# Kernel tuning notes

Measured on AMD Instinct MI355X. Metric: run time of the kernel, lower is better.

Reference implementation:

```python
import jax, jax.numpy as jnp
import numpy as np

N = 100000
E = 1600000
DIN = 128
H = 64
OUT_CLAMP = 10.0


def setup_inputs() -> dict:
    key = jax.random.key(0)
    ks = jax.random.split(key, 8)
    x = jax.random.normal(ks[0], (N, DIN), dtype=jnp.float32)
    edge_index = jax.random.randint(ks[1], (2, E), 0, N, dtype=jnp.int64)
    edge_weight = jax.random.uniform(ks[2], (E,), dtype=jnp.float32)
    # learned params (glorot-ish scale)
    W1 = jax.random.normal(ks[3], (DIN, H), dtype=jnp.float32) / np.sqrt(DIN)
    b1 = jnp.zeros((H,), dtype=jnp.float32)
    W2 = jax.random.normal(ks[4], (H, H), dtype=jnp.float32) / np.sqrt(H)
    b2 = jnp.zeros((H,), dtype=jnp.float32)
    fc_w = jax.random.normal(ks[5], (H, 1), dtype=jnp.float32) / np.sqrt(H)
    fc_b = jnp.zeros((1,), dtype=jnp.float32)
    return {"x": x, "edge_index": edge_index, "edge_weight": edge_weight,
            "W1": W1, "b1": b1, "W2": W2, "b2": b2, "fc_w": fc_w, "fc_b": fc_b}


def _gcn_conv(h, src, dst, norm, W, b, n_nodes):
    # h: [N, Fin] -> [N, Fout]. PyG GCNConv: linear, gather at source,
    # scale by symmetric norm, scatter-add at target, add bias.
    hw = h @ W                                   # [N, Fout]
    msg = hw[src] * norm[:, None]                # [E+N, Fout]
    out = jax.ops.segment_sum(msg, dst, num_segments=n_nodes)
    return out + b


def _gcn_norm(edge_index, edge_weight, n_nodes):
    # add self-loops with weight 1, compute deg^-1/2 symmetric norm
    loop = jnp.arange(n_nodes, dtype=edge_index.dtype)
    src = jnp.concatenate([edge_index[0], loop])
    dst = jnp.concatenate([edge_index[1], loop])
    ew = jnp.concatenate([edge_weight, jnp.ones((n_nodes,), edge_weight.dtype)])
    deg = jax.ops.segment_sum(ew, dst, num_segments=n_nodes)
    dis = jnp.where(deg > 0, jax.lax.rsqrt(jnp.maximum(deg, 1e-12)), 0.0)
    norm = dis[src] * ew * dis[dst]
    return src, dst, norm


def reference(x, edge_index, edge_weight, W1, b1, W2, b2, fc_w, fc_b):
    src, dst, norm = _gcn_norm(edge_index, edge_weight, N)
    h = _gcn_conv(x, src, dst, norm, W1, b1, N)
    h = _gcn_conv(h, src, dst, norm, W2, b2, N)
    out = h @ fc_w + fc_b                        # [N, 1]
    out = jnp.clip(out, 0.0, OUT_CLAMP)
    return jnp.round(out)
```

## Files before the change

### kernel.cpp

```cpp
#include <hip/hip_runtime.h>

#define DIN 128
#define BINW 128
#define BINSHIFT 7
#define NB_MAX 1024
#define CHUNK 8192


__global__ void precompute_kernel(const float* __restrict__ W1, const float* __restrict__ b1,
                                  const float* __restrict__ W2, const float* __restrict__ b2,
                                  const float* __restrict__ fcw, const float* __restrict__ fcb,
                                  double* __restrict__ w1f, double* __restrict__ cvals,
                                  unsigned* __restrict__ binCnt, int nb) {
    const int t = threadIdx.x;
    if (blockIdx.x > 0) {
        int i = (blockIdx.x - 1) * 256 + t;
        if (i < nb) binCnt[i] = 0u;
        return;
    }
    __shared__ double sw2f[64];
    if (t < 64) {
        double s = 0.0;
        for (int j = 0; j < 64; j++) s += (double)W2[t * 64 + j] * (double)fcw[j];
        sw2f[t] = s;
    }
    __syncthreads();
    if (t < 128) {
        double s = 0.0;
        for (int j = 0; j < 64; j++) s += (double)W1[t * 64 + j] * sw2f[j];
        w1f[t] = s;
    }
    if (t == 128) {
        double c1 = 0.0, c0 = (double)fcb[0];
        for (int j = 0; j < 64; j++) {
            c1 += (double)b1[j] * sw2f[j];
            c0 += (double)b2[j] * (double)fcw[j];
        }
        cvals[0] = c0;
        cvals[1] = c1;
    }
}

__global__ __launch_bounds__(256) void hist_gemv_kernel(
        const int* __restrict__ dst, const float* __restrict__ X,
        const double* __restrict__ w1f, unsigned* __restrict__ binCnt,
        double2* __restrict__ pk1, int n, int e, int nb, int hblk) {
    __shared__ unsigned cnt[NB_MAX];
    const int blk = blockIdx.x;
    const int t = threadIdx.x;
    if (blk < hblk) {
        for (int b = t; b < nb; b += 256) cnt[b] = 0u;
        __syncthreads();
        const long base = (long)blk * CHUNK;
        for (int k = 0; k < CHUNK / 256; k++) {
            long i = base + k * 256 + t;
            if (i < e) atomicAdd(&cnt[dst[i] >> BINSHIFT], 1u);
        }
        __syncthreads();
        for (int b = t; b < nb; b += 256) {
            unsigned c = cnt[b];
            if (c) atomicAdd(&binCnt[b], c);
        }
        return;
    }
    long g = (long)(blk - hblk) * 256 + t;
    int row = (int)(g >> 6);
    int lane = (int)(g & 63);
    if (row >= n) return;
    float2 x = *(const float2*)(X + (long)row * DIN + 2 * lane);
    double v = (double)x.x * w1f[2 * lane] + (double)x.y * w1f[2 * lane + 1];
#pragma unroll
    for (int off = 32; off > 0; off >>= 1) v += __shfl_down(v, off, 64);
    if (lane == 0) pk1[row].x = v;
}

__global__ void scan_kernel(const unsigned* __restrict__ binCnt,
                            unsigned* __restrict__ binBase,
                            unsigned* __restrict__ binCur, int nb) {
    __shared__ unsigned part[256];
    const int t = threadIdx.x;
    unsigned loc[4];
    unsigned s = 0;
#pragma unroll
    for (int k = 0; k < 4; k++) {
        int idx = t * 4 + k;
        unsigned v = (idx < nb) ? binCnt[idx] : 0u;
        loc[k] = s;
        s += v;
    }
    part[t] = s;
    __syncthreads();
    if (t == 0) {
        unsigned run = 0;
        for (int j = 0; j < 256; j++) { unsigned v = part[j]; part[j] = run; run += v; }
    }
    __syncthreads();
    unsigned p = part[t];
#pragma unroll
    for (int k = 0; k < 4; k++) {
        int idx = t * 4 + k;
        if (idx < nb) { binBase[idx] = p + loc[k]; binCur[idx] = p + loc[k]; }
    }
    if (t == 255) binBase[nb] = p + s;
}

__global__ __launch_bounds__(256) void binscatter_kernel(
        const int* __restrict__ src, const int* __restrict__ dst,
        const float* __restrict__ ew, unsigned* __restrict__ binCur,
        uint2* __restrict__ binned, int e, int nb) {
    __shared__ unsigned cnt[NB_MAX];
    __shared__ unsigned rb[NB_MAX];
    const int blk = blockIdx.x;
    const int t = threadIdx.x;
    for (int b = t; b < nb; b += 256) cnt[b] = 0u;
    __syncthreads();
    const long base = (long)blk * CHUNK;
    for (int k = 0; k < CHUNK / 256; k++) {
        long i = base + k * 256 + t;
        if (i < e) atomicAdd(&cnt[dst[i] >> BINSHIFT], 1u);
    }
    __syncthreads();
    for (int b = t; b < nb; b += 256) {
        unsigned c = cnt[b];
        rb[b] = c ? atomicAdd(&binCur[b], c) : 0u;
        cnt[b] = 0u;
    }
    __syncthreads();
    for (int k = 0; k < CHUNK / 256; k++) {
        long i = base + k * 256 + t;
        if (i < e) {
            int d = dst[i];
            int b = d >> BINSHIFT;
            unsigned p = rb[b] + atomicAdd(&cnt[b], 1u);
            binned[p] = uint2{(unsigned)src[i] | ((unsigned)(d & (BINW - 1)) << 20),
                              __float_as_uint(ew[i])};
        }
    }
}

__global__ __launch_bounds__(256) void setup_kernel(
        const uint2* __restrict__ binned, const unsigned* __restrict__ binBase,
        const double* __restrict__ cvals,
        double2* __restrict__ pk1, double2* __restrict__ pk2, int n) {
    __shared__ float ws[BINW];
    const int b = blockIdx.x;
    const int t = threadIdx.x;
    if (t < BINW) ws[t] = 0.0f;
    __syncthreads();
    const unsigned s0 = binBase[b], s1 = binBase[b + 1];
    for (unsigned i = s0 + t; i < s1; i += 256) {
        uint2 v = binned[i];
        atomicAdd(&ws[v.x >> 20], __uint_as_float(v.y));
    }
    __syncthreads();
    if (t < BINW) {
        int node = b * BINW + t;
        if (node < n) {
            float d = 1.0f + ws[t];
            float di = (d > 0.0f) ? (1.0f / sqrtf(fmaxf(d, 1e-12f))) : 0.0f;
            double qv = pk1[node].x;
            pk1[node] = double2{qv, (double)di};
            pk2[node] = double2{cvals[1] + (double)(di * di) * qv, (double)di};
        }
    }
}

__global__ __launch_bounds__(256) void spmv1_kernel(
        const uint2* __restrict__ binned, const unsigned* __restrict__ binBase,
        const double2* __restrict__ pk1, double2* __restrict__ pk2, int n) {
    __shared__ double acc[BINW];
    const int b = blockIdx.x;
    const int t = threadIdx.x;
    if (t < BINW) acc[t] = 0.0;
    __syncthreads();
    const unsigned s0 = binBase[b], s1 = binBase[b + 1];
    for (unsigned tile = s0; tile < s1; tile += 1024) {
        uint2 ee[4];
        double2 aa[4];
        bool ok[4];
#pragma unroll
        for (int k = 0; k < 4; k++) {
            unsigned idx = tile + t + k * 256u;
            ok[k] = (idx < s1);
            if (ok[k]) ee[k] = binned[idx];
        }
#pragma unroll
        for (int k = 0; k < 4; k++)
            if (ok[k]) aa[k] = pk1[ee[k].x & 0xFFFFFu];
#pragma unroll
        for (int k = 0; k < 4; k++)
            if (ok[k]) {
                float nm = (float)aa[k].y * __uint_as_float(ee[k].y);
                atomicAdd(&acc[ee[k].x >> 20], (double)nm * aa[k].x);
            }
    }
    __syncthreads();
    if (t < BINW) {
        int node = b * BINW + t;
        if (node < n) {
            double2 me = pk2[node];
            pk2[node].x = me.x + me.y * acc[t];
        }
    }
}

__global__ __launch_bounds__(256) void spmv2_head_kernel(
        const uint2* __restrict__ binned, const unsigned* __restrict__ binBase,
        const double2* __restrict__ pk2, const double* __restrict__ cvals,
        float* __restrict__ out, int n) {
    __shared__ double acc[BINW];
    const int b = blockIdx.x;
    const int t = threadIdx.x;
    if (t < BINW) acc[t] = 0.0;
    __syncthreads();
    const unsigned s0 = binBase[b], s1 = binBase[b + 1];
    for (unsigned tile = s0; tile < s1; tile += 1024) {
        uint2 ee[4];
        double2 aa[4];
        bool ok[4];
#pragma unroll
        for (int k = 0; k < 4; k++) {
            unsigned idx = tile + t + k * 256u;
            ok[k] = (idx < s1);
            if (ok[k]) ee[k] = binned[idx];
        }
#pragma unroll
        for (int k = 0; k < 4; k++)
            if (ok[k]) aa[k] = pk2[ee[k].x & 0xFFFFFu];
#pragma unroll
        for (int k = 0; k < 4; k++)
            if (ok[k]) {
                float nm = (float)aa[k].y * __uint_as_float(ee[k].y);
                atomicAdd(&acc[ee[k].x >> 20], (double)nm * aa[k].x);
            }
    }
    __syncthreads();
    if (t < BINW) {
        int node = b * BINW + t;
        if (node < n) {
            double2 me = pk2[node];
            float di = (float)me.y;
            double u = cvals[0] + (double)(di * di) * me.x + me.y * acc[t];
            float o = (float)u;
            o = fminf(fmaxf(o, 0.0f), 10.0f);
            out[node] = rintf(o);
        }
    }
}

extern "C" void kernel_launch(void* const* d_in, const int* in_sizes, int n_in,
                              void* d_out, int out_size, void* d_ws, size_t ws_size,
                              hipStream_t stream) {
    const float* x   = (const float*)d_in[0];
    const int*   eix = (const int*)d_in[1];
    const float* ew  = (const float*)d_in[2];
    const float* W1  = (const float*)d_in[3];
    const float* b1  = (const float*)d_in[4];
    const float* W2  = (const float*)d_in[5];
    const float* b2  = (const float*)d_in[6];
    const float* fcw = (const float*)d_in[7];
    const float* fcb = (const float*)d_in[8];
    float* out = (float*)d_out;

    const int n = in_sizes[0] / DIN;
    const int e = in_sizes[2];
    const int* src = eix;
    const int* dst = eix + e;
    const int nb = (n + BINW - 1) / BINW;

    auto al = [](size_t v) { return (v + 63) & ~(size_t)63; };
    double* ws = (double*)d_ws;
    size_t o = 0;
    double*   w1f    = ws + o; o += al(DIN);
    double*   cvals  = ws + o; o += al(2);
    double2*  pk1    = (double2*)(ws + o); o += al((size_t)n * 2);
    double2*  pk2    = (double2*)(ws + o); o += al((size_t)n * 2);
    unsigned* binCnt = (unsigned*)(ws + o); o += al(((size_t)nb + 1) / 2);
    unsigned* binBase= (unsigned*)(ws + o); o += al(((size_t)nb + 2) / 2);
    unsigned* binCur = (unsigned*)(ws + o); o += al(((size_t)nb + 1) / 2);
    uint2*    binned = (uint2*)(ws + o);

    const int hblk = (e + CHUNK - 1) / CHUNK;
    const int gemvblk = (n + 3) / 4;
    const int zblk = (nb + 255) / 256;

    precompute_kernel<<<1 + zblk, 256, 0, stream>>>(W1, b1, W2, b2, fcw, fcb,
                                                    w1f, cvals, binCnt, nb);
    hist_gemv_kernel<<<hblk + gemvblk, 256, 0, stream>>>(dst, x, w1f, binCnt,
                                                         pk1, n, e, nb, hblk);
    scan_kernel<<<1, 256, 0, stream>>>(binCnt, binBase, binCur, nb);
    binscatter_kernel<<<hblk, 256, 0, stream>>>(src, dst, ew, binCur, binned, e, nb);
    setup_kernel<<<nb, 256, 0, stream>>>(binned, binBase, cvals, pk1, pk2, n);
    spmv1_kernel<<<nb, 256, 0, stream>>>(binned, binBase, pk1, pk2, n);
    spmv2_head_kernel<<<nb, 256, 0, stream>>>(binned, binBase, pk2, cvals, out, n);
}
```

Measured before the change: 213.8 us.

## Replace atomic bin cursors with per-chunk histogram table and column scan

The histogram pass now writes each chunk's per-bin counts to a table instead of atomically accumulating global bin counts. A new kernel scans each bin's column across chunks to produce per-chunk write offsets and totals. The scatter pass then skips its own recount and global atomics, reading precomputed bases directly, and runs with 1024-thread blocks. This trades a second read of dst and contended global atomics for an extra kernel launch and a chunk-by-bin table (about 196x782 entries) in workspace.

Result: faster. 191.4 us (-10.5%).

```diff
diff --git a/kernel.cpp b/kernel.cpp
--- a/kernel.cpp
+++ b/kernel.cpp
@@ -10,14 +10,8 @@
 __global__ void precompute_kernel(const float* __restrict__ W1, const float* __restrict__ b1,
                                   const float* __restrict__ W2, const float* __restrict__ b2,
                                   const float* __restrict__ fcw, const float* __restrict__ fcb,
-                                  double* __restrict__ w1f, double* __restrict__ cvals,
-                                  unsigned* __restrict__ binCnt, int nb) {
-    const int t = threadIdx.x;
-    if (blockIdx.x > 0) {
-        int i = (blockIdx.x - 1) * 256 + t;
-        if (i < nb) binCnt[i] = 0u;
-        return;
-    }
+                                  double* __restrict__ w1f, double* __restrict__ cvals) {
+    const int t = threadIdx.x;
     __shared__ double sw2f[64];
     if (t < 64) {
         double s = 0.0;
@@ -43,7 +37,7 @@
 
 __global__ __launch_bounds__(256) void hist_gemv_kernel(
         const int* __restrict__ dst, const float* __restrict__ X,
-        const double* __restrict__ w1f, unsigned* __restrict__ binCnt,
+        const double* __restrict__ w1f, unsigned* __restrict__ histT,
         double2* __restrict__ pk1, int n, int e, int nb, int hblk) {
     __shared__ unsigned cnt[NB_MAX];
     const int blk = blockIdx.x;
@@ -57,10 +51,8 @@
             if (i < e) atomicAdd(&cnt[dst[i] >> BINSHIFT], 1u);
         }
         __syncthreads();
-        for (int b = t; b < nb; b += 256) {
-            unsigned c = cnt[b];
-            if (c) atomicAdd(&binCnt[b], c);
-        }
+        for (int b = t; b < nb; b += 256)
+            histT[(long)blk * nb + b] = cnt[b];
         return;
     }
     long g = (long)(blk - hblk) * 256 + t;
@@ -74,9 +66,30 @@
     if (lane == 0) pk1[row].x = v;
 }
 
+__global__ __launch_bounds__(256) void binscan_kernel(
+        const unsigned* __restrict__ histT, unsigned* __restrict__ chunkOfsT,
+        unsigned* __restrict__ binCnt, int nb, int hblk) {
+    int gw = (int)((blockIdx.x * 256 + threadIdx.x) >> 6);
+    int l = threadIdx.x & 63;
+    if (gw >= nb) return;
+    unsigned carry = 0u;
+    for (int c0 = 0; c0 < hblk; c0 += 64) {
+        int c = c0 + l;
+        unsigned v = (c < hblk) ? histT[(long)c * nb + gw] : 0u;
+        unsigned s = v;
+#pragma unroll
+        for (int off = 1; off < 64; off <<= 1) {
+            unsigned u = __shfl_up(s, off, 64);
+            if (l >= off) s += u;
+        }
+        if (c < hblk) chunkOfsT[(long)c * nb + gw] = carry + s - v;
+        carry += (unsigned)__shfl((int)s, 63, 64);
+    }
+    if (l == 0) binCnt[gw] = carry;
+}
+
 __global__ void scan_kernel(const unsigned* __restrict__ binCnt,
-                            unsigned* __restrict__ binBase,
-                            unsigned* __restrict__ binCur, int nb) {
+                            unsigned* __restrict__ binBase, int nb) {
     __shared__ unsigned part[256];
     const int t = threadIdx.x;
     unsigned loc[4];
@@ -99,39 +112,33 @@
 #pragma unroll
     for (int k = 0; k < 4; k++) {
         int idx = t * 4 + k;
-        if (idx < nb) { binBase[idx] = p + loc[k]; binCur[idx] = p + loc[k]; }
+        if (idx < nb) binBase[idx] = p + loc[k];
     }
     if (t == 255) binBase[nb] = p + s;
 }
 
-__global__ __launch_bounds__(256) void binscatter_kernel(
+__global__ __launch_bounds__(1024) void binscatter_kernel(
         const int* __restrict__ src, const int* __restrict__ dst,
-        const float* __restrict__ ew, unsigned* __restrict__ binCur,
+        const float* __restrict__ ew, const unsigned* __restrict__ binBase,
+        const unsigned* __restrict__ chunkOfsT,
         uint2* __restrict__ binned, int e, int nb) {
     __shared__ unsigned cnt[NB_MAX];
-    __shared__ unsigned rb[NB_MAX];
-    const int blk = blockIdx.x;
-    const int t = threadIdx.x;
-    for (int b = t; b < nb; b += 256) cnt[b] = 0u;
-    __syncthreads();
-    const long base = (long)blk * CHUNK;
-    for (int k = 0; k < CHUNK / 256; k++) {
-        long i = base + k * 256 + t;
-        if (i < e) atomicAdd(&cnt[dst[i] >> BINSHIFT], 1u);
-    }
-    __syncthreads();
-    for (int b = t; b < nb; b += 256) {
-        unsigned c = cnt[b];
-        rb[b] = c ? atomicAdd(&binCur[b], c) : 0u;
+    __shared__ unsigned sbase[NB_MAX];
+    const int c = blockIdx.x;
+    const int t = threadIdx.x;
+    for (int b = t; b < nb; b += 1024) {
         cnt[b] = 0u;
-    }
-    __syncthreads();
-    for (int k = 0; k < CHUNK / 256; k++) {
-        long i = base + k * 256 + t;
+        sbase[b] = binBase[b] + chunkOfsT[(long)c * nb + b];
+    }
+    __syncthreads();
+    const long base = (long)c * CHUNK;
+#pragma unroll
+    for (int k = 0; k < CHUNK / 1024; k++) {
+        long i = base + k * 1024 + t;
         if (i < e) {
             int d = dst[i];
             int b = d >> BINSHIFT;
-            unsigned p = rb[b] + atomicAdd(&cnt[b], 1u);
+            unsigned p = sbase[b] + atomicAdd(&cnt[b], 1u);
             binned[p] = uint2{(unsigned)src[i] | ((unsigned)(d & (BINW - 1)) << 20),
                               __float_as_uint(ew[i])};
         }
@@ -267,29 +274,31 @@
     const int* src = eix;
     const int* dst = eix + e;
     const int nb = (n + BINW - 1) / BINW;
+    const int hblk = (e + CHUNK - 1) / CHUNK;
 
     auto al = [](size_t v) { return (v + 63) & ~(size_t)63; };
     double* ws = (double*)d_ws;
     size_t o = 0;
-    double*   w1f    = ws + o; o += al(DIN);
-    double*   cvals  = ws + o; o += al(2);
-    double2*  pk1    = (double2*)(ws + o); o += al((size_t)n * 2);
-    double2*  pk2    = (double2*)(ws + o); o += al((size_t)n * 2);
-    unsigned* binCnt = (unsigned*)(ws + o); o += al(((size_t)nb + 1) / 2);
-    unsigned* binBase= (unsigned*)(ws + o); o += al(((size_t)nb + 2) / 2);
-    unsigned* binCur = (unsigned*)(ws + o); o += al(((size_t)nb + 1) / 2);
-    uint2*    binned = (uint2*)(ws + o);
-
-    const int hblk = (e + CHUNK - 1) / CHUNK;
+    double*   w1f     = ws + o; o += al(DIN);
+    double*   cvals   = ws + o; o += al(2);
+    double2*  pk1     = (double2*)(ws + o); o += al((size_t)n * 2);
+    double2*  pk2     = (double2*)(ws + o); o += al((size_t)n * 2);
+    unsigned* binCnt  = (unsigned*)(ws + o); o += al(((size_t)nb + 1) / 2);
+    unsigned* binBase = (unsigned*)(ws + o); o += al(((size_t)nb + 2) / 2);
+    unsigned* histT   = (unsigned*)(ws + o); o += al(((size_t)nb * hblk + 1) / 2);
+    unsigned* chunkOfsT = (unsigned*)(ws + o); o += al(((size_t)nb * hblk + 1) / 2);
+    uint2*    binned  = (uint2*)(ws + o);
+
     const int gemvblk = (n + 3) / 4;
-    const int zblk = (nb + 255) / 256;
-
-    precompute_kernel<<<1 + zblk, 256, 0, stream>>>(W1, b1, W2, b2, fcw, fcb,
-                                                    w1f, cvals, binCnt, nb);
-    hist_gemv_kernel<<<hblk + gemvblk, 256, 0, stream>>>(dst, x, w1f, binCnt,
+    const int bsblk = (nb * 64 + 255) / 256;
+
+    precompute_kernel<<<1, 256, 0, stream>>>(W1, b1, W2, b2, fcw, fcb, w1f, cvals);
+    hist_gemv_kernel<<<hblk + gemvblk, 256, 0, stream>>>(dst, x, w1f, histT,
                                                          pk1, n, e, nb, hblk);
-    scan_kernel<<<1, 256, 0, stream>>>(binCnt, binBase, binCur, nb);
-    binscatter_kernel<<<hblk, 256, 0, stream>>>(src, dst, ew, binCur, binned, e, nb);
+    binscan_kernel<<<bsblk, 256, 0, stream>>>(histT, chunkOfsT, binCnt, nb, hblk);
+    scan_kernel<<<1, 256, 0, stream>>>(binCnt, binBase, nb);
+    binscatter_kernel<<<hblk, 1024, 0, stream>>>(src, dst, ew, binBase, chunkOfsT,
+                                                 binned, e, nb);
     setup_kernel<<<nb, 256, 0, stream>>>(binned, binBase, cvals, pk1, pk2, n);
     spmv1_kernel<<<nb, 256, 0, stream>>>(binned, binBase, pk1, pk2, n);
     spmv2_head_kernel<<<nb, 256, 0, stream>>>(binned, binBase, pk2, cvals, out, n);
```
